# Optimization experiments

Hardware: AMD Instinct MI355X
Metric: run time of the kernel (lower is better)

## Reference

```python
import jax, jax.numpy as jnp
import numpy as np

VOCAB = 50000
DIM = 768


def setup_inputs() -> dict:
    key = jax.random.key(0)
    k1, k2, k3, k4 = jax.random.split(key, 4)
    token = jax.random.randint(k1, (32, 512), 0, VOCAB, dtype=jnp.int64)
    need_mapper = jax.random.randint(k2, (VOCAB,), 0, 2, dtype=jnp.int32)
    bert_embedding = jax.random.normal(k3, (VOCAB, DIM), dtype=jnp.float32)
    mapper_w = jax.random.normal(k4, (DIM, DIM), dtype=jnp.float32) * (1.0 / np.sqrt(DIM))
    mapper_b = jnp.zeros((DIM,), dtype=jnp.float32)
    return {
        "token": token,
        "need_mapper": need_mapper,
        "bert_embedding": bert_embedding,
        "mapper_w": mapper_w,
        "mapper_b": mapper_b,
    }


def reference(token, need_mapper, bert_embedding, mapper_w, mapper_b):
    # Gather: [B, S, D] -- irregular access into the embedding table.
    vecs = bert_embedding[token]
    # Conditional mapper (vectorized over all tokens; selected by per-id mask).
    mapped = jnp.einsum("bsd,de->bse", vecs, mapper_w) + mapper_b
    need = need_mapper[token].astype(bool)  # [B, S]
    return jnp.where(need[..., None], mapped, vecs)
```

## Files before the change

### kernel.cpp

```cpp
#include <hip/hip_runtime.h>
#include <stdint.h>
#include <stddef.h>

#define DIM 768

typedef short short8 __attribute__((ext_vector_type(8)));
typedef float f32x4 __attribute__((ext_vector_type(4)));

__device__ inline unsigned short f2bf_rne(float f) {
    union { float f; unsigned u; } x; x.f = f;
    unsigned r = x.u + 0x7fffu + ((x.u >> 16) & 1u);
    return (unsigned short)(r >> 16);
}

__device__ inline void gload_lds16(const void* g, void* l) {
    __builtin_amdgcn_global_load_lds((const __attribute__((address_space(1))) void*)g,
                                     (__attribute__((address_space(3))) void*)l, 16, 0, 0);
}

__global__ __launch_bounds__(256) void convw_kernel(
    const float* __restrict__ w, unsigned short* __restrict__ Bt)
{
    __shared__ unsigned short t[64][65];
    const int k0 = blockIdx.x * 64, n0 = blockIdx.y * 64;
    const int tid = threadIdx.x;
#pragma unroll
    for (int p = 0; p < 16; ++p) {
        int e = p * 256 + tid;
        int r = e >> 6, c = e & 63;
        t[c][r] = f2bf_rne(w[(size_t)(k0 + r) * DIM + n0 + c]);
    }
    __syncthreads();
#pragma unroll
    for (int p = 0; p < 16; ++p) {
        int e = p * 256 + tid;
        int r = e >> 6, c = e & 63;
        Bt[(size_t)(n0 + r) * DIM + k0 + c] = t[r][c];
    }
}

__global__ __launch_bounds__(256) void fused_gemm_kernel(
    const int* __restrict__ token,
    const int* __restrict__ need_mapper,
    const float* __restrict__ emb,
    const unsigned short* __restrict__ Bt,
    const float* __restrict__ bias,
    float* __restrict__ out)
{
    __shared__ float          As[2][128 * 32];
    __shared__ unsigned short Bs[2][128 * 32];
    __shared__ int tok_s[128];
    __shared__ int flag_s[128];

    const int tid  = threadIdx.x;
    const int wave = tid >> 6;
    const int lane = tid & 63;
    const int quad = lane >> 4;
    const int l15  = lane & 15;
    const int wm   = wave >> 1;
    const int wn   = wave & 1;
    const int tile_m = blockIdx.x;
    const int tile_n = blockIdx.y;

    if (tid < 128) {
        int t = token[tile_m * 128 + tid];
        tok_s[tid]  = t;
        flag_s[tid] = need_mapper[t];
    }
    __syncthreads();

    const int r8 = tid >> 3;
    const int c8 = tid & 7;
    const float* pA[4];
#pragma unroll
    for (int j = 0; j < 4; ++j) {
        int r = j * 32 + r8;
        pA[j] = emb + (size_t)tok_s[r] * DIM + ((c8 ^ (r & 7)) << 2);
    }
    const unsigned short* pB = Bt + (size_t)(tile_n * 128 + (tid >> 2)) * DIM + (tid & 3) * 8;

#define STAGE(b, kk) do { \
    _Pragma("unroll") \
    for (int j = 0; j < 4; ++j) \
        gload_lds16(pA[j] + (kk), &As[(b)][(wave * 8) * 32 + j * 32 * 32]); \
    gload_lds16(pB + (kk),                   &Bs[(b)][wave * 512]); \
    gload_lds16(pB + (kk) + (size_t)64 * DIM, &Bs[(b)][2048 + wave * 512]); \
} while (0)

    f32x4 acc[4][4] = {};

#define COMPUTE(b) do { \
    short8 af[4], bf[4]; \
    _Pragma("unroll") \
    for (int i = 0; i < 4; ++i) { \
        const int m = wm * 64 + i * 16 + l15; \
        const float* row = &As[(b)][m << 5]; \
        f32x4 a0 = *(const f32x4*)(row + ((((quad << 1)    ) ^ (m & 7)) << 2)); \
        f32x4 a1 = *(const f32x4*)(row + ((((quad << 1) + 1) ^ (m & 7)) << 2)); \
        unsigned u0 = __float_as_uint(a0[0]) + 0x8000u; \
        unsigned u1 = __float_as_uint(a0[1]) + 0x8000u; \
        unsigned u2 = __float_as_uint(a0[2]) + 0x8000u; \
        unsigned u3 = __float_as_uint(a0[3]) + 0x8000u; \
        unsigned u4 = __float_as_uint(a1[0]) + 0x8000u; \
        unsigned u5 = __float_as_uint(a1[1]) + 0x8000u; \
        unsigned u6 = __float_as_uint(a1[2]) + 0x8000u; \
        unsigned u7 = __float_as_uint(a1[3]) + 0x8000u; \
        union { int i4[4]; short8 s; } pk; \
        pk.i4[0] = __builtin_amdgcn_perm(u1, u0, 0x07060302); \
        pk.i4[1] = __builtin_amdgcn_perm(u3, u2, 0x07060302); \
        pk.i4[2] = __builtin_amdgcn_perm(u5, u4, 0x07060302); \
        pk.i4[3] = __builtin_amdgcn_perm(u7, u6, 0x07060302); \
        af[i] = pk.s; \
    } \
    _Pragma("unroll") \
    for (int j = 0; j < 4; ++j) \
        bf[j] = *(const short8*)(&Bs[(b)][(wn * 64 + j * 16 + l15) * 32 + quad * 8]); \
    _Pragma("unroll") \
    for (int i = 0; i < 4; ++i) \
        _Pragma("unroll") \
        for (int j = 0; j < 4; ++j) \
            acc[i][j] = __builtin_amdgcn_mfma_f32_16x16x32_bf16(af[i], bf[j], acc[i][j], 0, 0, 0); \
} while (0)

    STAGE(0, 0);
    int cur = 0;
    for (int kk = 32; kk < DIM; kk += 32) {
        STAGE(cur ^ 1, kk);
        asm volatile("s_waitcnt vmcnt(6)" ::: "memory");
        __builtin_amdgcn_sched_barrier(0);
        __builtin_amdgcn_s_barrier();
        COMPUTE(cur);
        asm volatile("s_waitcnt lgkmcnt(0)" ::: "memory");
        __builtin_amdgcn_sched_barrier(0);
        __builtin_amdgcn_s_barrier();
        cur ^= 1;
    }
    asm volatile("s_waitcnt vmcnt(0)" ::: "memory");
    __builtin_amdgcn_sched_barrier(0);
    __builtin_amdgcn_s_barrier();
    COMPUTE(cur);

    const int colg = tile_n * 128 + wn * 64 + l15;
    float bv[4];
#pragma unroll
    for (int j = 0; j < 4; ++j) bv[j] = bias[colg + j * 16];

#pragma unroll
    for (int i = 0; i < 4; ++i) {
#pragma unroll
        for (int r = 0; r < 4; ++r) {
            const int lrow = wm * 64 + i * 16 + quad * 4 + r;
            const int gm   = tile_m * 128 + lrow;
            float* orow = out + (size_t)gm * DIM + colg;
            if (flag_s[lrow]) {
#pragma unroll
                for (int j = 0; j < 4; ++j)
                    orow[j * 16] = acc[i][j][r] + bv[j];
            } else {
                const float* erow = emb + (size_t)tok_s[lrow] * DIM + colg;
#pragma unroll
                for (int j = 0; j < 4; ++j)
                    orow[j * 16] = erow[j * 16];
            }
        }
    }
#undef STAGE
#undef COMPUTE
}

extern "C" void kernel_launch(void* const* d_in, const int* in_sizes, int n_in,
                              void* d_out, int out_size, void* d_ws, size_t ws_size,
                              hipStream_t stream)
{
    const int*   token       = (const int*)d_in[0];
    const int*   need_mapper = (const int*)d_in[1];
    const float* emb         = (const float*)d_in[2];
    const float* w           = (const float*)d_in[3];
    const float* bias        = (const float*)d_in[4];
    float* out = (float*)d_out;

    const int ntok = in_sizes[0];

    unsigned short* Bt = (unsigned short*)d_ws;

    convw_kernel<<<dim3(DIM / 64, DIM / 64), dim3(256), 0, stream>>>(w, Bt);
    fused_gemm_kernel<<<dim3(ntok / 128, DIM / 128), dim3(256), 0, stream>>>(
        token, need_mapper, emb, Bt, bias, out);
}
```

Baseline: 244.6 us.

## Prefetch A into registers, convert to bf16 before LDS, halve M tile

A rows now go from global memory into registers two steps ahead. They are converted to bf16 and written to LDS as packed shorts, replacing the direct fp32 global-to-LDS loads that were converted on every compute pass. The M tile shrinks from 128 to 64 rows, which doubles the grid, and launch bounds request 4 blocks per CU. The B tile gains an XOR swizzle to match. The aim is to cut LDS footprint and per-MFMA conversion work and to raise occupancy. In exchange, each B tile is reloaded by twice as many blocks and the loop uses hand-tuned waitcnt scheduling.

```diff
diff --git a/kernel.cpp b/kernel.cpp
--- a/kernel.cpp
+++ b/kernel.cpp
@@ -39,7 +39,7 @@
     }
 }
 
-__global__ __launch_bounds__(256) void fused_gemm_kernel(
+__global__ __launch_bounds__(256, 4) void fused_gemm_kernel(
     const int* __restrict__ token,
     const int* __restrict__ need_mapper,
     const float* __restrict__ emb,
@@ -47,10 +47,10 @@
     const float* __restrict__ bias,
     float* __restrict__ out)
 {
-    __shared__ float          As[2][128 * 32];
+    __shared__ unsigned short As[2][64 * 32];
     __shared__ unsigned short Bs[2][128 * 32];
-    __shared__ int tok_s[128];
-    __shared__ int flag_s[128];
+    __shared__ int tok_s[64];
+    __shared__ int flag_s[64];
 
     const int tid  = threadIdx.x;
     const int wave = tid >> 6;
@@ -62,82 +62,111 @@
     const int tile_m = blockIdx.x;
     const int tile_n = blockIdx.y;
 
-    if (tid < 128) {
-        int t = token[tile_m * 128 + tid];
+    if (tid < 64) {
+        int t = token[tile_m * 64 + tid];
         tok_s[tid]  = t;
         flag_s[tid] = need_mapper[t];
     }
     __syncthreads();
 
-    const int r8 = tid >> 3;
-    const int c8 = tid & 7;
-    const float* pA[4];
-#pragma unroll
-    for (int j = 0; j < 4; ++j) {
-        int r = j * 32 + r8;
-        pA[j] = emb + (size_t)tok_s[r] * DIM + ((c8 ^ (r & 7)) << 2);
-    }
-    const unsigned short* pB = Bt + (size_t)(tile_n * 128 + (tid >> 2)) * DIM + (tid & 3) * 8;
-
-#define STAGE(b, kk) do { \
+    const int rA_row = tid >> 2;
+    const int rA_c   = tid & 3;
+    const float* pA  = emb + (size_t)tok_s[rA_row] * DIM + rA_c * 8;
+    const int wAidx  = rA_row * 32 + ((rA_c ^ ((rA_row >> 1) & 3)) << 3);
+
+    const int rb = tid >> 2, sb = tid & 3;
+    const unsigned short* pB0 = Bt + (size_t)(tile_n * 128 + rb) * DIM + ((sb ^ ((rb >> 1) & 3)) << 3);
+    const unsigned short* pB1 = Bt + (size_t)(tile_n * 128 + 64 + rb) * DIM + ((sb ^ (((64 + rb) >> 1) & 3)) << 3);
+
+#define GLOADB(b, kk) do { \
+    gload_lds16(pB0 + (kk), &Bs[(b)][wave * 512]); \
+    gload_lds16(pB1 + (kk), &Bs[(b)][2048 + wave * 512]); \
+} while (0)
+
+#define WRITEA(b, ra, rb_) do { \
+    unsigned u0 = __float_as_uint((ra)[0]) + 0x8000u; \
+    unsigned u1 = __float_as_uint((ra)[1]) + 0x8000u; \
+    unsigned u2 = __float_as_uint((ra)[2]) + 0x8000u; \
+    unsigned u3 = __float_as_uint((ra)[3]) + 0x8000u; \
+    unsigned u4 = __float_as_uint((rb_)[0]) + 0x8000u; \
+    unsigned u5 = __float_as_uint((rb_)[1]) + 0x8000u; \
+    unsigned u6 = __float_as_uint((rb_)[2]) + 0x8000u; \
+    unsigned u7 = __float_as_uint((rb_)[3]) + 0x8000u; \
+    union { int i4[4]; short8 s; } pk; \
+    pk.i4[0] = __builtin_amdgcn_perm(u1, u0, 0x07060302); \
+    pk.i4[1] = __builtin_amdgcn_perm(u3, u2, 0x07060302); \
+    pk.i4[2] = __builtin_amdgcn_perm(u5, u4, 0x07060302); \
+    pk.i4[3] = __builtin_amdgcn_perm(u7, u6, 0x07060302); \
+    *(short8*)(&As[(b)][wAidx]) = pk.s; \
+} while (0)
+
+    f32x4 acc[2][4] = {};
+
+#define COMPUTE(b) do { \
+    short8 af[2], bf[4]; \
     _Pragma("unroll") \
-    for (int j = 0; j < 4; ++j) \
-        gload_lds16(pA[j] + (kk), &As[(b)][(wave * 8) * 32 + j * 32 * 32]); \
-    gload_lds16(pB + (kk),                   &Bs[(b)][wave * 512]); \
-    gload_lds16(pB + (kk) + (size_t)64 * DIM, &Bs[(b)][2048 + wave * 512]); \
-} while (0)
-
-    f32x4 acc[4][4] = {};
-
-#define COMPUTE(b) do { \
-    short8 af[4], bf[4]; \
-    _Pragma("unroll") \
-    for (int i = 0; i < 4; ++i) { \
-        const int m = wm * 64 + i * 16 + l15; \
-        const float* row = &As[(b)][m << 5]; \
-        f32x4 a0 = *(const f32x4*)(row + ((((quad << 1)    ) ^ (m & 7)) << 2)); \
-        f32x4 a1 = *(const f32x4*)(row + ((((quad << 1) + 1) ^ (m & 7)) << 2)); \
-        unsigned u0 = __float_as_uint(a0[0]) + 0x8000u; \
-        unsigned u1 = __float_as_uint(a0[1]) + 0x8000u; \
-        unsigned u2 = __float_as_uint(a0[2]) + 0x8000u; \
-        unsigned u3 = __float_as_uint(a0[3]) + 0x8000u; \
-        unsigned u4 = __float_as_uint(a1[0]) + 0x8000u; \
-        unsigned u5 = __float_as_uint(a1[1]) + 0x8000u; \
-        unsigned u6 = __float_as_uint(a1[2]) + 0x8000u; \
-        unsigned u7 = __float_as_uint(a1[3]) + 0x8000u; \
-        union { int i4[4]; short8 s; } pk; \
-        pk.i4[0] = __builtin_amdgcn_perm(u1, u0, 0x07060302); \
-        pk.i4[1] = __builtin_amdgcn_perm(u3, u2, 0x07060302); \
-        pk.i4[2] = __builtin_amdgcn_perm(u5, u4, 0x07060302); \
-        pk.i4[3] = __builtin_amdgcn_perm(u7, u6, 0x07060302); \
-        af[i] = pk.s; \
+    for (int i = 0; i < 2; ++i) { \
+        const int m = wm * 32 + i * 16 + l15; \
+        af[i] = *(const short8*)(&As[(b)][m * 32 + ((quad ^ ((m >> 1) & 3)) << 3)]); \
     } \
     _Pragma("unroll") \
-    for (int j = 0; j < 4; ++j) \
-        bf[j] = *(const short8*)(&Bs[(b)][(wn * 64 + j * 16 + l15) * 32 + quad * 8]); \
+    for (int j = 0; j < 4; ++j) { \
+        const int n = wn * 64 + j * 16 + l15; \
+        bf[j] = *(const short8*)(&Bs[(b)][n * 32 + ((quad ^ ((n >> 1) & 3)) << 3)]); \
+    } \
     _Pragma("unroll") \
-    for (int i = 0; i < 4; ++i) \
+    for (int i = 0; i < 2; ++i) \
         _Pragma("unroll") \
         for (int j = 0; j < 4; ++j) \
             acc[i][j] = __builtin_amdgcn_mfma_f32_16x16x32_bf16(af[i], bf[j], acc[i][j], 0, 0, 0); \
 } while (0)
 
-    STAGE(0, 0);
+#define ITER_BODY(T, RCa, RCb, RDa, RDb) do { \
+    GLOADB(cur ^ 1, ((T) + 1) * 32); \
+    __builtin_amdgcn_sched_barrier(0); \
+    RDa = *(const f32x4*)(pA + ((T) + 2) * 32); \
+    RDb = *(const f32x4*)(pA + ((T) + 2) * 32 + 4); \
+    COMPUTE(cur); \
+    WRITEA(cur ^ 1, RCa, RCb); \
+    asm volatile("s_waitcnt vmcnt(2)" ::: "memory"); \
+    __builtin_amdgcn_sched_barrier(0); \
+    asm volatile("s_waitcnt lgkmcnt(0)" ::: "memory"); \
+    __builtin_amdgcn_sched_barrier(0); \
+    __builtin_amdgcn_s_barrier(); \
+    cur ^= 1; \
+} while (0)
+
+    f32x4 rTa, rTb, rA0a, rA0b, rA1a, rA1b;
+
+    rTa = *(const f32x4*)(pA);
+    rTb = *(const f32x4*)(pA + 4);
+    GLOADB(0, 0);
+    __builtin_amdgcn_sched_barrier(0);
+    rA0a = *(const f32x4*)(pA + 32);
+    rA0b = *(const f32x4*)(pA + 36);
+    WRITEA(0, rTa, rTb);
+    asm volatile("s_waitcnt vmcnt(2)" ::: "memory");
+    __builtin_amdgcn_sched_barrier(0);
+    asm volatile("s_waitcnt lgkmcnt(0)" ::: "memory");
+    __builtin_amdgcn_sched_barrier(0);
+    __builtin_amdgcn_s_barrier();
+
     int cur = 0;
-    for (int kk = 32; kk < DIM; kk += 32) {
-        STAGE(cur ^ 1, kk);
-        asm volatile("s_waitcnt vmcnt(6)" ::: "memory");
-        __builtin_amdgcn_sched_barrier(0);
-        __builtin_amdgcn_s_barrier();
-        COMPUTE(cur);
-        asm volatile("s_waitcnt lgkmcnt(0)" ::: "memory");
-        __builtin_amdgcn_sched_barrier(0);
-        __builtin_amdgcn_s_barrier();
-        cur ^= 1;
-    }
+#pragma unroll 1
+    for (int t = 0; t < 22; t += 2) {
+        ITER_BODY(t,     rA0a, rA0b, rA1a, rA1b);
+        ITER_BODY(t + 1, rA1a, rA1b, rA0a, rA0b);
+    }
+    GLOADB(cur ^ 1, 23 * 32);
+    __builtin_amdgcn_sched_barrier(0);
+    COMPUTE(cur);
+    WRITEA(cur ^ 1, rA0a, rA0b);
     asm volatile("s_waitcnt vmcnt(0)" ::: "memory");
     __builtin_amdgcn_sched_barrier(0);
+    asm volatile("s_waitcnt lgkmcnt(0)" ::: "memory");
+    __builtin_amdgcn_sched_barrier(0);
     __builtin_amdgcn_s_barrier();
+    cur ^= 1;
     COMPUTE(cur);
 
     const int colg = tile_n * 128 + wn * 64 + l15;
@@ -146,11 +175,11 @@
     for (int j = 0; j < 4; ++j) bv[j] = bias[colg + j * 16];
 
 #pragma unroll
-    for (int i = 0; i < 4; ++i) {
+    for (int i = 0; i < 2; ++i) {
 #pragma unroll
         for (int r = 0; r < 4; ++r) {
-            const int lrow = wm * 64 + i * 16 + quad * 4 + r;
-            const int gm   = tile_m * 128 + lrow;
+            const int lrow = wm * 32 + i * 16 + quad * 4 + r;
+            const int gm   = tile_m * 64 + lrow;
             float* orow = out + (size_t)gm * DIM + colg;
             if (flag_s[lrow]) {
 #pragma unroll
@@ -164,8 +193,10 @@
             }
         }
     }
-#undef STAGE
+#undef GLOADB
+#undef WRITEA
 #undef COMPUTE
+#undef ITER_BODY
 }
 
 extern "C" void kernel_launch(void* const* d_in, const int* in_sizes, int n_in,
@@ -184,6 +215,6 @@
     unsigned short* Bt = (unsigned short*)d_ws;
 
     convw_kernel<<<dim3(DIM / 64, DIM / 64), dim3(256), 0, stream>>>(w, Bt);
-    fused_gemm_kernel<<<dim3(ntok / 128, DIM / 128), dim3(256), 0, stream>>>(
+    fused_gemm_kernel<<<dim3(ntok / 64, DIM / 128), dim3(256), 0, stream>>>(
         token, need_mapper, emb, Bt, bias, out);
 }
```

After: 252.5 us. 3.2% more time.
